# Kernel tuning notes

Hardware: AMD Instinct MI355X
Metric: run time of the kernel (lower is better)

Reference implementation:

```python
import jax, jax.numpy as jnp
import numpy as np

B, R, IN, OUT = 32, 4, 1024, 1024
PI_MIX, SIGMA1, SIGMA2 = 0.5, 1.0, 0.1


def setup_inputs() -> dict:
    key = jax.random.key(0)
    ks = jax.random.split(key, 7)
    return {
        "x": jax.random.normal(ks[0], (B, IN), dtype=jnp.float32),
        "mu": jax.random.normal(ks[1], (IN, OUT), dtype=jnp.float32),
        "ro": jax.random.normal(ks[2], (IN, OUT), dtype=jnp.float32),
        "mu_bias": jax.random.normal(ks[3], (1, OUT), dtype=jnp.float32),
        "ro_bias": jax.random.normal(ks[4], (1, OUT), dtype=jnp.float32),
        "eps": jax.random.normal(ks[5], (B, R, IN, OUT), dtype=jnp.float32),
        "eps_bias": jax.random.normal(ks[6], (B, R, OUT), dtype=jnp.float32),
    }


def _gaussian(v, m, s):
    # pdf, clamped like the torch code
    bell = jnp.exp(-(v - m) ** 2 / (2.0 * s ** 2)) / (jnp.sqrt(2.0 * jnp.pi) * s)
    return jnp.clip(bell, 1e-10, 10.0)


def _mixture(v):
    return PI_MIX * _gaussian(v, 0.0, SIGMA1) + (1.0 - PI_MIX) * _gaussian(v, 0.0, SIGMA2)


def reference(x, mu, ro, mu_bias, ro_bias, eps, eps_bias):
    sigma = jnp.log1p(jnp.exp(ro))              # softplus, (IN, OUT)
    sigma_b = jnp.log1p(jnp.exp(ro_bias))       # (1, OUT)
    weights = eps * sigma + mu                  # (B, R, IN, OUT)
    bias = eps_bias * sigma_b + mu_bias         # (B, R, OUT)
    denom = x.shape[0] * R
    log_prior = (jnp.log(_mixture(weights)).sum() + jnp.log(_mixture(bias)).sum()) / denom
    log_p_weights = (jnp.log(_gaussian(weights, mu, sigma)).sum()
                     + jnp.log(_gaussian(bias, mu_bias, sigma_b)).sum()) / denom
    # out[b, r] = x[b] @ weights[b, r] + bias[b, r]; mean over r
    out = (jnp.einsum('bi,brio->bro', x, weights) + bias).mean(axis=1)  # (B, OUT)
    return out, log_prior, log_p_weights
```

## Files before the change

### kernel.cpp

```cpp
#include <hip/hip_runtime.h>
#include <math.h>

#define B_    32
#define R_    4
#define IN_   1024
#define OUT_  1024
#define S_    16
#define CHUNK (IN_ / S_)
#define NPRE  ((size_t)IN_ * OUT_ + OUT_)

#define C_HALF_LOG_2PI 0.9189385332046727f
#define INV_SQRT_2PI   0.3989422804014327f
#define INV_SQRT_2PI_S 3.9894228040143270f
#define LOG_MIN       -23.025850929940457f
#define LOG_MAX        2.3025850929940460f

__device__ __forceinline__ float softplus_f(float x) {
    return fmaxf(x, 0.0f) + log1pf(__expf(-fabsf(x)));
}

__global__ void init_kernel(float* __restrict__ out) {
    int idx = blockIdx.x * 256 + threadIdx.x;
    if (idx < B_ * OUT_ + 2) out[idx] = 0.0f;
}

__global__ void precomp_kernel(const float* __restrict__ ro,
                               const float* __restrict__ ro_bias,
                               float* __restrict__ sig,
                               float* __restrict__ lpb) {
    size_t idx = (size_t)blockIdx.x * 256 + threadIdx.x;
    if (idx >= NPRE) return;
    float rv = (idx < (size_t)IN_ * OUT_) ? ro[idx] : ro_bias[idx - (size_t)IN_ * OUT_];
    float sg = softplus_f(rv);
    sig[idx] = sg;
    lpb[idx] = -C_HALF_LOG_2PI - __logf(sg);
}

#define PROC(E, M, SG, LB, ACC)                                              \
    {                                                                        \
        float w  = fmaf((E), (SG), (M));                                     \
        (ACC)    = fmaf(xv, w, (ACC));                                       \
        float t  = -0.5f * w * w;                                            \
        float g1 = fmaxf(__expf(t)          * INV_SQRT_2PI,   1e-10f);       \
        float g2 = fmaxf(__expf(100.0f * t) * INV_SQRT_2PI_S, 1e-10f);       \
        smix += __logf(0.5f * (g1 + g2));                                    \
        float lw = fmaf((E) * (E), -0.5f, (LB));                             \
        slpw += fminf(fmaxf(lw, LOG_MIN), LOG_MAX);                          \
    }

template <bool USE_WS>
__global__ __launch_bounds__(256)
void main_kernel(const float* __restrict__ x,
                 const float* __restrict__ mu,
                 const float* __restrict__ ro,
                 const float* __restrict__ mu_bias,
                 const float* __restrict__ ro_bias,
                 const float* __restrict__ eps,
                 const float* __restrict__ eps_bias,
                 const float* __restrict__ sig_ws,
                 const float* __restrict__ lpb_ws,
                 float* __restrict__ out) {
    const int tid = threadIdx.x;
    const int bid = blockIdx.x;
    const int s   = bid & (S_ - 1);
    const int r   = (bid >> 4) & (R_ - 1);
    const int b   = bid >> 6;
    const int i0  = s * CHUNK;

    __shared__ float xs[CHUNK];
    if (tid < CHUNK) xs[tid] = x[b * IN_ + i0 + tid];
    __syncthreads();

    const size_t row0 = ((size_t)(b * R_ + r) * IN_ + i0) * OUT_;
    const float4* eps4 = (const float4*)(eps + row0) + tid;
    const float4* mu4  = (const float4*)(mu + (size_t)i0 * OUT_) + tid;
    const float4* ro4  = (const float4*)(ro + (size_t)i0 * OUT_) + tid;
    const float4* sig4 = USE_WS ? (const float4*)(sig_ws + (size_t)i0 * OUT_) + tid : nullptr;
    const float4* lpb4 = USE_WS ? (const float4*)(lpb_ws + (size_t)i0 * OUT_) + tid : nullptr;

    float4 acc = {0.f, 0.f, 0.f, 0.f};
    float smix = 0.f, slpw = 0.f;

    for (int ii = 0; ii < CHUNK; ++ii) {
        const int stride = ii * (OUT_ / 4);
        float  xv = xs[ii];
        float4 e  = eps4[stride];
        float4 m  = mu4[stride];
        float4 sg, lb;
        if (USE_WS) {
            sg = sig4[stride];
            lb = lpb4[stride];
        } else {
            float4 rr = ro4[stride];
            sg.x = softplus_f(rr.x); lb.x = -C_HALF_LOG_2PI - __logf(sg.x);
            sg.y = softplus_f(rr.y); lb.y = -C_HALF_LOG_2PI - __logf(sg.y);
            sg.z = softplus_f(rr.z); lb.z = -C_HALF_LOG_2PI - __logf(sg.z);
            sg.w = softplus_f(rr.w); lb.w = -C_HALF_LOG_2PI - __logf(sg.w);
        }
        PROC(e.x, m.x, sg.x, lb.x, acc.x);
        PROC(e.y, m.y, sg.y, lb.y, acc.y);
        PROC(e.z, m.z, sg.z, lb.z, acc.z);
        PROC(e.w, m.w, sg.w, lb.w, acc.w);
    }

    if (s == 0) {
        float4 eb = *((const float4*)(eps_bias + (size_t)(b * R_ + r) * OUT_) + tid);
        float4 mb = *((const float4*)mu_bias + tid);
        float4 sgb, lbb;
        if (USE_WS) {
            sgb = *((const float4*)(sig_ws + (size_t)IN_ * OUT_) + tid);
            lbb = *((const float4*)(lpb_ws + (size_t)IN_ * OUT_) + tid);
        } else {
            float4 rb = *((const float4*)ro_bias + tid);
            sgb.x = softplus_f(rb.x); lbb.x = -C_HALF_LOG_2PI - __logf(sgb.x);
            sgb.y = softplus_f(rb.y); lbb.y = -C_HALF_LOG_2PI - __logf(sgb.y);
            sgb.z = softplus_f(rb.z); lbb.z = -C_HALF_LOG_2PI - __logf(sgb.z);
            sgb.w = softplus_f(rb.w); lbb.w = -C_HALF_LOG_2PI - __logf(sgb.w);
        }
        float xv = 1.0f;
        PROC(eb.x, mb.x, sgb.x, lbb.x, acc.x);
        PROC(eb.y, mb.y, sgb.y, lbb.y, acc.y);
        PROC(eb.z, mb.z, sgb.z, lbb.z, acc.z);
        PROC(eb.w, mb.w, sgb.w, lbb.w, acc.w);
    }

    float* outp = out + (size_t)b * OUT_ + tid * 4;
    atomicAdd(outp + 0, acc.x * 0.25f);
    atomicAdd(outp + 1, acc.y * 0.25f);
    atomicAdd(outp + 2, acc.z * 0.25f);
    atomicAdd(outp + 3, acc.w * 0.25f);

    for (int off = 32; off > 0; off >>= 1) {
        smix += __shfl_down(smix, off, 64);
        slpw += __shfl_down(slpw, off, 64);
    }
    __shared__ float red[8];
    const int wave = tid >> 6, lane = tid & 63;
    if (lane == 0) { red[wave] = smix; red[4 + wave] = slpw; }
    __syncthreads();
    if (tid == 0) {
        float sm = red[0] + red[1] + red[2] + red[3];
        float sl = red[4] + red[5] + red[6] + red[7];
        atomicAdd(out + B_ * OUT_ + 0, sm * (1.0f / 128.0f));
        atomicAdd(out + B_ * OUT_ + 1, sl * (1.0f / 128.0f));
    }
}

extern "C" void kernel_launch(void* const* d_in, const int* in_sizes, int n_in,
                              void* d_out, int out_size, void* d_ws, size_t ws_size,
                              hipStream_t stream) {
    const float* x       = (const float*)d_in[0];
    const float* mu      = (const float*)d_in[1];
    const float* ro      = (const float*)d_in[2];
    const float* mu_bias = (const float*)d_in[3];
    const float* ro_bias = (const float*)d_in[4];
    const float* eps     = (const float*)d_in[5];
    const float* eps_b   = (const float*)d_in[6];
    float* out = (float*)d_out;

    const bool use_ws = ws_size >= 2 * NPRE * sizeof(float);
    float* sig_ws = (float*)d_ws;
    float* lpb_ws = sig_ws + NPRE;

    init_kernel<<<(B_ * OUT_ + 2 + 255) / 256, 256, 0, stream>>>(out);

    if (use_ws) {
        precomp_kernel<<<(int)((NPRE + 255) / 256), 256, 0, stream>>>(ro, ro_bias, sig_ws, lpb_ws);
        main_kernel<true><<<B_ * R_ * S_, 256, 0, stream>>>(
            x, mu, ro, mu_bias, ro_bias, eps, eps_b, sig_ws, lpb_ws, out);
    } else {
        main_kernel<false><<<B_ * R_ * S_, 256, 0, stream>>>(
            x, mu, ro, mu_bias, ro_bias, eps, eps_b, nullptr, nullptr, out);
    }
}
```

Measured before the change: 760.7 us.

## Factor log-sigma sum out of inner loop and use native exp2/log2 intrinsics

Rewrites the log-likelihood so the per-element log(sigma) term is pulled out of the main loop. Its sum is computed once in the precompute kernel and added as a constant, which removes the per-element lpb workspace array and its memory stream. The mixture-prior math now uses base-2 exp/log hardware intrinsics with folded constants, eps is loaded with nontemporal hints, and the loop is unrolled by 4. The trade-off is dropping the per-element clamp on log_p (equivalent only if it never triggers) and a changed float accumulation order.

Measured after the change: 784.2 us. 1.03x slower.

```diff
diff --git a/kernel.cpp b/kernel.cpp
--- a/kernel.cpp
+++ b/kernel.cpp
@@ -9,43 +9,61 @@
 #define CHUNK (IN_ / S_)
 #define NPRE  ((size_t)IN_ * OUT_ + OUT_)
 
-#define C_HALF_LOG_2PI 0.9189385332046727f
-#define INV_SQRT_2PI   0.3989422804014327f
-#define INV_SQRT_2PI_S 3.9894228040143270f
-#define LOG_MIN       -23.025850929940457f
-#define LOG_MAX        2.3025850929940460f
+typedef float f4 __attribute__((ext_vector_type(4)));
+
+#define C_HALF_LOG_2PI 0.9189385332046727
+#define LN2            0.6931471805599453f
+#define NHL2E         -0.7213475204444817f
+#define NHL2E_S       -72.13475204444817f
+#define K1            -2.3257550f
+#define K2             0.9961798f
 
 __device__ __forceinline__ float softplus_f(float x) {
     return fmaxf(x, 0.0f) + log1pf(__expf(-fabsf(x)));
 }
 
-__global__ void init_kernel(float* __restrict__ out) {
+__global__ void init_kernel(float* __restrict__ out, float* __restrict__ slog) {
     int idx = blockIdx.x * 256 + threadIdx.x;
     if (idx < B_ * OUT_ + 2) out[idx] = 0.0f;
+    if (idx == 0 && slog) *slog = 0.0f;
 }
 
 __global__ void precomp_kernel(const float* __restrict__ ro,
                                const float* __restrict__ ro_bias,
                                float* __restrict__ sig,
-                               float* __restrict__ lpb) {
+                               float* __restrict__ slog) {
     size_t idx = (size_t)blockIdx.x * 256 + threadIdx.x;
-    if (idx >= NPRE) return;
-    float rv = (idx < (size_t)IN_ * OUT_) ? ro[idx] : ro_bias[idx - (size_t)IN_ * OUT_];
-    float sg = softplus_f(rv);
-    sig[idx] = sg;
-    lpb[idx] = -C_HALF_LOG_2PI - __logf(sg);
+    float lg2 = 0.0f;
+    if (idx < NPRE) {
+        float rv = (idx < (size_t)IN_ * OUT_) ? ro[idx] : ro_bias[idx - (size_t)IN_ * OUT_];
+        float sg = softplus_f(rv);
+        sig[idx] = sg;
+        lg2 = __builtin_amdgcn_logf(sg);
+    }
+    for (int off = 32; off > 0; off >>= 1) lg2 += __shfl_down(lg2, off, 64);
+    __shared__ float red[4];
+    int wave = threadIdx.x >> 6, lane = threadIdx.x & 63;
+    if (lane == 0) red[wave] = lg2;
+    __syncthreads();
+    if (threadIdx.x == 0)
+        atomicAdd(slog, (red[0] + red[1] + red[2] + red[3]) * LN2);
 }
 
-#define PROC(E, M, SG, LB, ACC)                                              \
-    {                                                                        \
-        float w  = fmaf((E), (SG), (M));                                     \
-        (ACC)    = fmaf(xv, w, (ACC));                                       \
-        float t  = -0.5f * w * w;                                            \
-        float g1 = fmaxf(__expf(t)          * INV_SQRT_2PI,   1e-10f);       \
-        float g2 = fmaxf(__expf(100.0f * t) * INV_SQRT_2PI_S, 1e-10f);       \
-        smix += __logf(0.5f * (g1 + g2));                                    \
-        float lw = fmaf((E) * (E), -0.5f, (LB));                             \
-        slpw += fminf(fmaxf(lw, LOG_MIN), LOG_MAX);                          \
+#define PROC(E, M, SG, ACC)                                                   \
+    {                                                                         \
+        float w  = fmaf((E), (SG), (M));                                      \
+        (ACC)    = fmaf(xv, w, (ACC));                                        \
+        float t2 = w * w;                                                     \
+        float g1 = fmaxf(__builtin_amdgcn_exp2f(fmaf(t2, NHL2E,   K1)), 5e-11f); \
+        float g2 = fmaxf(__builtin_amdgcn_exp2f(fmaf(t2, NHL2E_S, K2)), 5e-11f); \
+        smix2 += __builtin_amdgcn_logf(g1 + g2);                              \
+        se2 = fmaf((E), (E), se2);                                            \
+    }
+
+#define SG_FALLBACK(RR, SG)                                                   \
+    {                                                                         \
+        (SG) = softplus_f(RR);                                                \
+        slg2 += __builtin_amdgcn_logf(SG);                                    \
     }
 
 template <bool USE_WS>
@@ -58,7 +76,7 @@
                  const float* __restrict__ eps,
                  const float* __restrict__ eps_bias,
                  const float* __restrict__ sig_ws,
-                 const float* __restrict__ lpb_ws,
+                 const float* __restrict__ slog_ws,
                  float* __restrict__ out) {
     const int tid = threadIdx.x;
     const int bid = blockIdx.x;
@@ -72,56 +90,50 @@
     __syncthreads();
 
     const size_t row0 = ((size_t)(b * R_ + r) * IN_ + i0) * OUT_;
-    const float4* eps4 = (const float4*)(eps + row0) + tid;
-    const float4* mu4  = (const float4*)(mu + (size_t)i0 * OUT_) + tid;
-    const float4* ro4  = (const float4*)(ro + (size_t)i0 * OUT_) + tid;
-    const float4* sig4 = USE_WS ? (const float4*)(sig_ws + (size_t)i0 * OUT_) + tid : nullptr;
-    const float4* lpb4 = USE_WS ? (const float4*)(lpb_ws + (size_t)i0 * OUT_) + tid : nullptr;
+    const f4* eps4 = (const f4*)(eps + row0) + tid;
+    const f4* mu4  = (const f4*)(mu + (size_t)i0 * OUT_) + tid;
+    const f4* ro4  = (const f4*)(ro + (size_t)i0 * OUT_) + tid;
+    const f4* sig4 = USE_WS ? (const f4*)(sig_ws + (size_t)i0 * OUT_) + tid : nullptr;
 
-    float4 acc = {0.f, 0.f, 0.f, 0.f};
-    float smix = 0.f, slpw = 0.f;
+    f4 acc = {0.f, 0.f, 0.f, 0.f};
+    float smix2 = 0.f, se2 = 0.f, slg2 = 0.f;
 
+#pragma unroll 4
     for (int ii = 0; ii < CHUNK; ++ii) {
         const int stride = ii * (OUT_ / 4);
-        float  xv = xs[ii];
-        float4 e  = eps4[stride];
-        float4 m  = mu4[stride];
-        float4 sg, lb;
+        float xv = xs[ii];
+        f4 e = __builtin_nontemporal_load(eps4 + stride);
+        f4 m = mu4[stride];
+        f4 sg;
         if (USE_WS) {
             sg = sig4[stride];
-            lb = lpb4[stride];
         } else {
-            float4 rr = ro4[stride];
-            sg.x = softplus_f(rr.x); lb.x = -C_HALF_LOG_2PI - __logf(sg.x);
-            sg.y = softplus_f(rr.y); lb.y = -C_HALF_LOG_2PI - __logf(sg.y);
-            sg.z = softplus_f(rr.z); lb.z = -C_HALF_LOG_2PI - __logf(sg.z);
-            sg.w = softplus_f(rr.w); lb.w = -C_HALF_LOG_2PI - __logf(sg.w);
+            f4 rr = ro4[stride];
+            SG_FALLBACK(rr.x, sg.x); SG_FALLBACK(rr.y, sg.y);
+            SG_FALLBACK(rr.z, sg.z); SG_FALLBACK(rr.w, sg.w);
         }
-        PROC(e.x, m.x, sg.x, lb.x, acc.x);
-        PROC(e.y, m.y, sg.y, lb.y, acc.y);
-        PROC(e.z, m.z, sg.z, lb.z, acc.z);
-        PROC(e.w, m.w, sg.w, lb.w, acc.w);
+        PROC(e.x, m.x, sg.x, acc.x);
+        PROC(e.y, m.y, sg.y, acc.y);
+        PROC(e.z, m.z, sg.z, acc.z);
+        PROC(e.w, m.w, sg.w, acc.w);
     }
 
     if (s == 0) {
-        float4 eb = *((const float4*)(eps_bias + (size_t)(b * R_ + r) * OUT_) + tid);
-        float4 mb = *((const float4*)mu_bias + tid);
-        float4 sgb, lbb;
+        f4 eb = *((const f4*)(eps_bias + (size_t)(b * R_ + r) * OUT_) + tid);
+        f4 mb = *((const f4*)mu_bias + tid);
+        f4 sgb;
         if (USE_WS) {
-            sgb = *((const float4*)(sig_ws + (size_t)IN_ * OUT_) + tid);
-            lbb = *((const float4*)(lpb_ws + (size_t)IN_ * OUT_) + tid);
+            sgb = *((const f4*)(sig_ws + (size_t)IN_ * OUT_) + tid);
         } else {
-            float4 rb = *((const float4*)ro_bias + tid);
-            sgb.x = softplus_f(rb.x); lbb.x = -C_HALF_LOG_2PI - __logf(sgb.x);
-            sgb.y = softplus_f(rb.y); lbb.y = -C_HALF_LOG_2PI - __logf(sgb.y);
-            sgb.z = softplus_f(rb.z); lbb.z = -C_HALF_LOG_2PI - __logf(sgb.z);
-            sgb.w = softplus_f(rb.w); lbb.w = -C_HALF_LOG_2PI - __logf(sgb.w);
+            f4 rb = *((const f4*)ro_bias + tid);
+            SG_FALLBACK(rb.x, sgb.x); SG_FALLBACK(rb.y, sgb.y);
+            SG_FALLBACK(rb.z, sgb.z); SG_FALLBACK(rb.w, sgb.w);
         }
         float xv = 1.0f;
-        PROC(eb.x, mb.x, sgb.x, lbb.x, acc.x);
-        PROC(eb.y, mb.y, sgb.y, lbb.y, acc.y);
-        PROC(eb.z, mb.z, sgb.z, lbb.z, acc.z);
-        PROC(eb.w, mb.w, sgb.w, lbb.w, acc.w);
+        PROC(eb.x, mb.x, sgb.x, acc.x);
+        PROC(eb.y, mb.y, sgb.y, acc.y);
+        PROC(eb.z, mb.z, sgb.z, acc.z);
+        PROC(eb.w, mb.w, sgb.w, acc.w);
     }
 
     float* outp = out + (size_t)b * OUT_ + tid * 4;
@@ -130,19 +142,25 @@
     atomicAdd(outp + 2, acc.z * 0.25f);
     atomicAdd(outp + 3, acc.w * 0.25f);
 
+    float lpw = fmaf(se2, -0.5f, USE_WS ? 0.0f : (-LN2 * slg2));
     for (int off = 32; off > 0; off >>= 1) {
-        smix += __shfl_down(smix, off, 64);
-        slpw += __shfl_down(slpw, off, 64);
+        smix2 += __shfl_down(smix2, off, 64);
+        lpw   += __shfl_down(lpw,   off, 64);
     }
     __shared__ float red[8];
     const int wave = tid >> 6, lane = tid & 63;
-    if (lane == 0) { red[wave] = smix; red[4 + wave] = slpw; }
+    if (lane == 0) { red[wave] = smix2; red[4 + wave] = lpw; }
     __syncthreads();
     if (tid == 0) {
         float sm = red[0] + red[1] + red[2] + red[3];
         float sl = red[4] + red[5] + red[6] + red[7];
-        atomicAdd(out + B_ * OUT_ + 0, sm * (1.0f / 128.0f));
+        atomicAdd(out + B_ * OUT_ + 0, sm * (LN2 / 128.0f));
         atomicAdd(out + B_ * OUT_ + 1, sl * (1.0f / 128.0f));
+        if (bid == 0) {
+            float c = -(float)((double)NPRE * C_HALF_LOG_2PI);
+            if (USE_WS) c -= *slog_ws;
+            atomicAdd(out + B_ * OUT_ + 1, c);
+        }
     }
 }
 
@@ -158,16 +176,18 @@
     const float* eps_b   = (const float*)d_in[6];
     float* out = (float*)d_out;
 
-    const bool use_ws = ws_size >= 2 * NPRE * sizeof(float);
-    float* sig_ws = (float*)d_ws;
-    float* lpb_ws = sig_ws + NPRE;
+    const bool use_ws = ws_size >= (NPRE + 1) * sizeof(float);
+    float* sig_ws  = (float*)d_ws;
+    float* slog_ws = sig_ws + NPRE;
 
-    init_kernel<<<(B_ * OUT_ + 2 + 255) / 256, 256, 0, stream>>>(out);
+    init_kernel<<<(B_ * OUT_ + 2 + 255) / 256, 256, 0, stream>>>(
+        out, use_ws ? slog_ws : nullptr);
 
     if (use_ws) {
-        precomp_kernel<<<(int)((NPRE + 255) / 256), 256, 0, stream>>>(ro, ro_bias, sig_ws, lpb_ws);
+        precomp_kernel<<<(int)((NPRE + 255) / 256), 256, 0, stream>>>(
+            ro, ro_bias, sig_ws, slog_ws);
         main_kernel<true><<<B_ * R_ * S_, 256, 0, stream>>>(
-            x, mu, ro, mu_bias, ro_bias, eps, eps_b, sig_ws, lpb_ws, out);
+            x, mu, ro, mu_bias, ro_bias, eps, eps_b, sig_ws, slog_ws, out);
     } else {
         main_kernel<false><<<B_ * R_ * S_, 256, 0, stream>>>(
             x, mu, ro, mu_bias, ro_bias, eps, eps_b, nullptr, nullptr, out);
```
